# Optimization experiments

Measured on AMD Instinct MI355X. Metric: run time of the kernel, lower is better.

Reference implementation:

```python
import jax, jax.numpy as jnp
import numpy as np

N, H, V = 2048, 2048, 32000

def setup_inputs() -> dict:
    key = jax.random.key(0)
    k1, k2, k3 = jax.random.split(key, 3)
    x = jax.random.normal(k1, (N, H), dtype=jnp.float32)
    y = jax.random.normal(k2, (N, V), dtype=jnp.float32)
    # nn.Linear default init: U(-1/sqrt(H), 1/sqrt(H))
    bound = 1.0 / np.sqrt(H)
    W = jax.random.uniform(k3, (V, H), dtype=jnp.float32, minval=-bound, maxval=bound)
    return {"x": x, "y": y, "W": W}

def reference(x, y, W):
    # logits = x @ W^T : [N, V]
    logits = jnp.einsum('nh,vh->nv', x, W)
    # MSE with 'mean' reduction over all elements
    diff = logits - y
    return jnp.mean(diff * diff)
```

## Files before the change

kernel.cpp:

```cpp
#include <hip/hip_runtime.h>

#define MDIM 2048
#define KDIM 2048
#define VDIM 32000
#define TILE 128
#define BK 32
#define LDAB (2 * KDIM)

typedef __bf16 bf16x8 __attribute__((ext_vector_type(8)));
typedef float f32x4 __attribute__((ext_vector_type(4)));

__device__ __forceinline__ unsigned short f32_to_bf16_rne(float f) {
    unsigned u = __float_as_uint(f);
    u += 0x7FFFu + ((u >> 16) & 1u);
    return (unsigned short)(u >> 16);
}

__global__ __launch_bounds__(256) void cast_inplace_rows_kernel(
        float* __restrict__ rows, float* zero_out) {
    if (zero_out && blockIdx.x == 0 && threadIdx.x == 0) *zero_out = 0.0f;
    float* frow = rows + (long)blockIdx.x * KDIM;
    const int t = threadIdx.x;
    const float4* p = reinterpret_cast<const float4*>(frow + t * 8);
    float4 a = p[0];
    float4 b = p[1];
    __syncthreads();
    union { unsigned short h[8]; uint4 u; } r;
    r.h[0] = f32_to_bf16_rne(a.x);
    r.h[1] = f32_to_bf16_rne(a.y);
    r.h[2] = f32_to_bf16_rne(a.z);
    r.h[3] = f32_to_bf16_rne(a.w);
    r.h[4] = f32_to_bf16_rne(b.x);
    r.h[5] = f32_to_bf16_rne(b.y);
    r.h[6] = f32_to_bf16_rne(b.z);
    r.h[7] = f32_to_bf16_rne(b.w);
    reinterpret_cast<uint4*>(frow)[t] = r.u;
}

__global__ __launch_bounds__(256) void gemm_mse_kernel(
        const unsigned short* __restrict__ A,
        const unsigned short* __restrict__ B,
        const float* __restrict__ Y,
        float* __restrict__ out) {
    __shared__ __align__(16) unsigned short As[TILE * BK];
    __shared__ __align__(16) unsigned short Bs[TILE * BK];

    const int tid  = threadIdx.x;
    const int lane = tid & 63;
    const int wave = tid >> 6;
    const int wr = (wave >> 1) * 64;
    const int wc = (wave & 1) * 64;
    const int m0 = lane & 15;
    const int q  = lane >> 4;

    const long rowBase = (long)blockIdx.x * TILE;
    const long colBase = (long)blockIdx.y * TILE;

    f32x4 acc[4][4];
#pragma unroll
    for (int i = 0; i < 4; ++i)
#pragma unroll
        for (int j = 0; j < 4; ++j)
            acc[i][j] = (f32x4){0.f, 0.f, 0.f, 0.f};

    const int l0 = tid;
    const int l1 = tid + 256;
    const unsigned short* ag0 = A + (rowBase + (l0 >> 2)) * LDAB + (l0 & 3) * 8;
    const unsigned short* ag1 = A + (rowBase + (l1 >> 2)) * LDAB + (l1 & 3) * 8;
    const unsigned short* bg0 = B + (colBase + (l0 >> 2)) * LDAB + (l0 & 3) * 8;
    const unsigned short* bg1 = B + (colBase + (l1 >> 2)) * LDAB + (l1 & 3) * 8;
    unsigned short* as0 = As + l0 * 8;
    unsigned short* as1 = As + l1 * 8;
    unsigned short* bs0 = Bs + l0 * 8;
    unsigned short* bs1 = Bs + l1 * 8;

    const unsigned short* arow = As + (wr + m0) * BK + q * 8;
    const unsigned short* brow = Bs + (wc + m0) * BK + q * 8;

    for (int kt = 0; kt < KDIM; kt += BK) {
        __syncthreads();
        __builtin_amdgcn_global_load_lds(
            (const __attribute__((address_space(1))) void*)(ag0 + kt),
            (__attribute__((address_space(3))) void*)as0, 16, 0, 0);
        __builtin_amdgcn_global_load_lds(
            (const __attribute__((address_space(1))) void*)(ag1 + kt),
            (__attribute__((address_space(3))) void*)as1, 16, 0, 0);
        __builtin_amdgcn_global_load_lds(
            (const __attribute__((address_space(1))) void*)(bg0 + kt),
            (__attribute__((address_space(3))) void*)bs0, 16, 0, 0);
        __builtin_amdgcn_global_load_lds(
            (const __attribute__((address_space(1))) void*)(bg1 + kt),
            (__attribute__((address_space(3))) void*)bs1, 16, 0, 0);
        __syncthreads();

        bf16x8 af[4], bfr[4];
#pragma unroll
        for (int i = 0; i < 4; ++i)
            af[i] = *(const bf16x8*)(const void*)(arow + i * 16 * BK);
#pragma unroll
        for (int j = 0; j < 4; ++j)
            bfr[j] = *(const bf16x8*)(const void*)(brow + j * 16 * BK);
#pragma unroll
        for (int i = 0; i < 4; ++i)
#pragma unroll
            for (int j = 0; j < 4; ++j)
                acc[i][j] = __builtin_amdgcn_mfma_f32_16x16x32_bf16(
                    af[i], bfr[j], acc[i][j], 0, 0, 0);
    }

    float sum = 0.f;
#pragma unroll
    for (int i = 0; i < 4; ++i) {
#pragma unroll
        for (int j = 0; j < 4; ++j) {
            long gr = rowBase + wr + i * 16 + q * 4;
            long gc = colBase + wc + j * 16 + m0;
            const float* yp = Y + gr * VDIM + gc;
#pragma unroll
            for (int r = 0; r < 4; ++r) {
                float d = acc[i][j][r] - yp[(long)r * VDIM];
                sum += d * d;
            }
        }
    }
    sum += __shfl_down(sum, 32);
    sum += __shfl_down(sum, 16);
    sum += __shfl_down(sum, 8);
    sum += __shfl_down(sum, 4);
    sum += __shfl_down(sum, 2);
    sum += __shfl_down(sum, 1);
    if (lane == 0)
        atomicAdd(out, sum * (1.0f / ((float)MDIM * (float)VDIM)));
}

extern "C" void kernel_launch(void* const* d_in, const int* in_sizes, int n_in,
                              void* d_out, int out_size, void* d_ws, size_t ws_size,
                              hipStream_t stream) {
    float* x = (float*)d_in[0];
    const float* y = (const float*)d_in[1];
    float* W = (float*)d_in[2];
    float* out = (float*)d_out;
    (void)d_ws; (void)ws_size;

    cast_inplace_rows_kernel<<<MDIM, 256, 0, stream>>>(x, out);
    cast_inplace_rows_kernel<<<VDIM, 256, 0, stream>>>(W, nullptr);

    dim3 grid(MDIM / TILE, VDIM / TILE);
    gemm_mse_kernel<<<grid, 256, 0, stream>>>(
        (const unsigned short*)x, (const unsigned short*)W, y, out);
}
```

Measured before the change: 846.8 us.

## Double K tile with XOR-swizzled LDS, batch cast rows, reduce per block

The GEMM K tile grows from 32 to 64, so each barrier pair now covers two MFMA sub-steps. The LDS layout uses an XOR swizzle on 16-byte segments to avoid bank conflicts on fragment reads. The cast kernel handles four rows per block, and the final MSE partial sums are reduced across waves in LDS so each block issues a single atomic. LDS use doubles and there is still no double buffering, so load latency stays exposed.

```diff
diff --git a/kernel.cpp b/kernel.cpp
--- a/kernel.cpp
+++ b/kernel.cpp
@@ -4,11 +4,12 @@
 #define KDIM 2048
 #define VDIM 32000
 #define TILE 128
-#define BK 32
+#define BK 64
 #define LDAB (2 * KDIM)
 
 typedef __bf16 bf16x8 __attribute__((ext_vector_type(8)));
 typedef float f32x4 __attribute__((ext_vector_type(4)));
+typedef unsigned short ushort_t;
 
 __device__ __forceinline__ unsigned short f32_to_bf16_rne(float f) {
     unsigned u = __float_as_uint(f);
@@ -16,25 +17,33 @@
     return (unsigned short)(u >> 16);
 }
 
-__global__ __launch_bounds__(256) void cast_inplace_rows_kernel(
+__global__ __launch_bounds__(256) void cast_inplace_rows4_kernel(
         float* __restrict__ rows, float* zero_out) {
     if (zero_out && blockIdx.x == 0 && threadIdx.x == 0) *zero_out = 0.0f;
-    float* frow = rows + (long)blockIdx.x * KDIM;
+    float* base = rows + (long)blockIdx.x * 4 * KDIM;
     const int t = threadIdx.x;
-    const float4* p = reinterpret_cast<const float4*>(frow + t * 8);
-    float4 a = p[0];
-    float4 b = p[1];
+    float4 v[8];
+#pragma unroll
+    for (int rr = 0; rr < 4; ++rr) {
+        const float4* p = reinterpret_cast<const float4*>(base + rr * KDIM + t * 8);
+        v[2 * rr]     = p[0];
+        v[2 * rr + 1] = p[1];
+    }
     __syncthreads();
-    union { unsigned short h[8]; uint4 u; } r;
-    r.h[0] = f32_to_bf16_rne(a.x);
-    r.h[1] = f32_to_bf16_rne(a.y);
-    r.h[2] = f32_to_bf16_rne(a.z);
-    r.h[3] = f32_to_bf16_rne(a.w);
-    r.h[4] = f32_to_bf16_rne(b.x);
-    r.h[5] = f32_to_bf16_rne(b.y);
-    r.h[6] = f32_to_bf16_rne(b.z);
-    r.h[7] = f32_to_bf16_rne(b.w);
-    reinterpret_cast<uint4*>(frow)[t] = r.u;
+#pragma unroll
+    for (int rr = 0; rr < 4; ++rr) {
+        union { unsigned short h[8]; uint4 u; } r;
+        float4 a = v[2 * rr], b = v[2 * rr + 1];
+        r.h[0] = f32_to_bf16_rne(a.x);
+        r.h[1] = f32_to_bf16_rne(a.y);
+        r.h[2] = f32_to_bf16_rne(a.z);
+        r.h[3] = f32_to_bf16_rne(a.w);
+        r.h[4] = f32_to_bf16_rne(b.x);
+        r.h[5] = f32_to_bf16_rne(b.y);
+        r.h[6] = f32_to_bf16_rne(b.z);
+        r.h[7] = f32_to_bf16_rne(b.w);
+        reinterpret_cast<uint4*>(base + rr * KDIM)[t] = r.u;
+    }
 }
 
 __global__ __launch_bounds__(256) void gemm_mse_kernel(
@@ -63,49 +72,57 @@
         for (int j = 0; j < 4; ++j)
             acc[i][j] = (f32x4){0.f, 0.f, 0.f, 0.f};
 
-    const int l0 = tid;
-    const int l1 = tid + 256;
-    const unsigned short* ag0 = A + (rowBase + (l0 >> 2)) * LDAB + (l0 & 3) * 8;
-    const unsigned short* ag1 = A + (rowBase + (l1 >> 2)) * LDAB + (l1 & 3) * 8;
-    const unsigned short* bg0 = B + (colBase + (l0 >> 2)) * LDAB + (l0 & 3) * 8;
-    const unsigned short* bg1 = B + (colBase + (l1 >> 2)) * LDAB + (l1 & 3) * 8;
-    unsigned short* as0 = As + l0 * 8;
-    unsigned short* as1 = As + l1 * 8;
-    unsigned short* bs0 = Bs + l0 * 8;
-    unsigned short* bs1 = Bs + l1 * 8;
+    const unsigned short* agp[4];
+    const unsigned short* bgp[4];
+    unsigned short* asp[4];
+    unsigned short* bsp[4];
+#pragma unroll
+    for (int s = 0; s < 4; ++s) {
+        int l = tid + 256 * s;
+        int row = l >> 3;
+        int segg = (l & 7) ^ (row & 7);
+        agp[s] = A + (rowBase + row) * LDAB + segg * 8;
+        bgp[s] = B + (colBase + row) * LDAB + segg * 8;
+        asp[s] = As + l * 8;
+        bsp[s] = Bs + l * 8;
+    }
 
-    const unsigned short* arow = As + (wr + m0) * BK + q * 8;
-    const unsigned short* brow = Bs + (wc + m0) * BK + q * 8;
+    const int sxor = m0 & 7;
+    const unsigned short* aRow = As + (wr + m0) * BK;
+    const unsigned short* bRow = Bs + (wc + m0) * BK;
+    const int off0 = ((q)     ^ sxor) * 8;
+    const int off1 = ((4 + q) ^ sxor) * 8;
 
     for (int kt = 0; kt < KDIM; kt += BK) {
         __syncthreads();
-        __builtin_amdgcn_global_load_lds(
-            (const __attribute__((address_space(1))) void*)(ag0 + kt),
-            (__attribute__((address_space(3))) void*)as0, 16, 0, 0);
-        __builtin_amdgcn_global_load_lds(
-            (const __attribute__((address_space(1))) void*)(ag1 + kt),
-            (__attribute__((address_space(3))) void*)as1, 16, 0, 0);
-        __builtin_amdgcn_global_load_lds(
-            (const __attribute__((address_space(1))) void*)(bg0 + kt),
-            (__attribute__((address_space(3))) void*)bs0, 16, 0, 0);
-        __builtin_amdgcn_global_load_lds(
-            (const __attribute__((address_space(1))) void*)(bg1 + kt),
-            (__attribute__((address_space(3))) void*)bs1, 16, 0, 0);
+#pragma unroll
+        for (int s = 0; s < 4; ++s) {
+            __builtin_amdgcn_global_load_lds(
+                (const __attribute__((address_space(1))) void*)(agp[s] + kt),
+                (__attribute__((address_space(3))) void*)asp[s], 16, 0, 0);
+            __builtin_amdgcn_global_load_lds(
+                (const __attribute__((address_space(1))) void*)(bgp[s] + kt),
+                (__attribute__((address_space(3))) void*)bsp[s], 16, 0, 0);
+        }
         __syncthreads();
 
-        bf16x8 af[4], bfr[4];
 #pragma unroll
-        for (int i = 0; i < 4; ++i)
-            af[i] = *(const bf16x8*)(const void*)(arow + i * 16 * BK);
+        for (int h = 0; h < 2; ++h) {
+            const int off = h ? off1 : off0;
+            bf16x8 af[4], bfr[4];
 #pragma unroll
-        for (int j = 0; j < 4; ++j)
-            bfr[j] = *(const bf16x8*)(const void*)(brow + j * 16 * BK);
-#pragma unroll
-        for (int i = 0; i < 4; ++i)
+            for (int i = 0; i < 4; ++i)
+                af[i] = *(const bf16x8*)(const void*)(aRow + i * 16 * BK + off);
 #pragma unroll
             for (int j = 0; j < 4; ++j)
-                acc[i][j] = __builtin_amdgcn_mfma_f32_16x16x32_bf16(
-                    af[i], bfr[j], acc[i][j], 0, 0, 0);
+                bfr[j] = *(const bf16x8*)(const void*)(bRow + j * 16 * BK + off);
+#pragma unroll
+            for (int i = 0; i < 4; ++i)
+#pragma unroll
+                for (int j = 0; j < 4; ++j)
+                    acc[i][j] = __builtin_amdgcn_mfma_f32_16x16x32_bf16(
+                        af[i], bfr[j], acc[i][j], 0, 0, 0);
+        }
     }
 
     float sum = 0.f;
@@ -129,8 +146,14 @@
     sum += __shfl_down(sum, 4);
     sum += __shfl_down(sum, 2);
     sum += __shfl_down(sum, 1);
-    if (lane == 0)
-        atomicAdd(out, sum * (1.0f / ((float)MDIM * (float)VDIM)));
+    __syncthreads();
+    float* red = (float*)(void*)As;
+    if (lane == 0) red[wave] = sum;
+    __syncthreads();
+    if (tid == 0) {
+        float t = (red[0] + red[1]) + (red[2] + red[3]);
+        atomicAdd(out, t * (1.0f / ((float)MDIM * (float)VDIM)));
+    }
 }
 
 extern "C" void kernel_launch(void* const* d_in, const int* in_sizes, int n_in,
@@ -142,8 +165,8 @@
     float* out = (float*)d_out;
     (void)d_ws; (void)ws_size;
 
-    cast_inplace_rows_kernel<<<MDIM, 256, 0, stream>>>(x, out);
-    cast_inplace_rows_kernel<<<VDIM, 256, 0, stream>>>(W, nullptr);
+    cast_inplace_rows4_kernel<<<MDIM / 4, 256, 0, stream>>>(x, out);
+    cast_inplace_rows4_kernel<<<VDIM / 4, 256, 0, stream>>>(W, nullptr);
 
     dim3 grid(MDIM / TILE, VDIM / TILE);
     gemm_mse_kernel<<<grid, 256, 0, stream>>>(
```

New measurement: 806.5 us. 4.7% less time.
